# Optimization experiments

Hardware: AMD Instinct MI355X
Metric: run time of the kernel (lower is better)

## Reference

```python
import jax, jax.numpy as jnp
import numpy as np

D_IN = 1024
D_OUT = 1024
NUM_HEADS = 16
HEAD_DIM = D_OUT // NUM_HEADS


def setup_inputs() -> dict:
    key = jax.random.key(0)
    ks = jax.random.split(key, 6)
    s = 1.0 / np.sqrt(D_IN)
    inputs = jax.random.normal(ks[0], (4, 2048, D_IN), dtype=jnp.float32)
    Wq = jax.random.uniform(ks[1], (D_IN, D_OUT), jnp.float32, -s, s)
    Wk = jax.random.uniform(ks[2], (D_IN, D_OUT), jnp.float32, -s, s)
    Wv = jax.random.uniform(ks[3], (D_IN, D_OUT), jnp.float32, -s, s)
    so = 1.0 / np.sqrt(D_OUT)
    Wo = jax.random.uniform(ks[4], (D_OUT, D_OUT), jnp.float32, -so, so)
    bo = jax.random.uniform(ks[5], (D_OUT,), jnp.float32, -so, so)
    return {"inputs": inputs, "Wq": Wq, "Wk": Wk, "Wv": Wv, "Wo": Wo, "bo": bo}


def reference(inputs, Wq, Wk, Wv, Wo, bo):
    b, n, _ = inputs.shape
    # projections -> [b, h, n, d]
    def split_heads(x):
        return x.reshape(b, n, NUM_HEADS, HEAD_DIM).transpose(0, 2, 1, 3)
    q = split_heads(inputs @ Wq)
    k = split_heads(inputs @ Wk)
    v = split_heads(inputs @ Wv)
    scores = jnp.einsum('bhqd,bhkd->bhqk', q, k) / np.sqrt(HEAD_DIM).astype(np.float32)
    causal = jnp.tril(jnp.ones((n, n), dtype=bool))  # True = keep
    scores = jnp.where(causal, scores, -jnp.inf)
    weights = jax.nn.softmax(scores, axis=-1)
    ctx = jnp.einsum('bhqk,bhkd->bhqd', weights, v)
    ctx = ctx.transpose(0, 2, 1, 3).reshape(b, n, D_OUT)
    return ctx @ Wo + bo
```

## Files before the change

### kernel.cpp

```cpp
#include <hip/hip_runtime.h>

typedef unsigned short u16;
typedef unsigned int u32;
typedef __attribute__((ext_vector_type(8))) short short8;
typedef __attribute__((ext_vector_type(4))) float floatx4;
typedef __attribute__((ext_vector_type(4))) unsigned short ushort4_t;
typedef __attribute__((ext_vector_type(4))) float float4_t;
typedef __attribute__((ext_vector_type(2))) unsigned int uint2_t;


__device__ __forceinline__ u16 f2bf(float f) {
  unsigned u = __builtin_bit_cast(unsigned, f);
  u += 0x7FFFu + ((u >> 16) & 1u);
  return (u16)(u >> 16);
}

__device__ __forceinline__ u32 pack_bf2(float a, float b) {
  u32 ua = __builtin_bit_cast(u32, a) + 0x8000u;
  u32 ub = __builtin_bit_cast(u32, b) + 0x8000u;
  return __builtin_amdgcn_perm(ua, ub, 0x07060302u);
}

__device__ __forceinline__ void gload_lds16(const void* g, void* l) {
  __builtin_amdgcn_global_load_lds(
      (const __attribute__((address_space(1))) void*)g,
      (__attribute__((address_space(3))) void*)l, 16, 0, 0);
}


__global__ void cvt_x(const float* __restrict__ src, u16* __restrict__ dst) {
  int i = blockIdx.x * 256 + threadIdx.x;
  float4_t f = ((const float4_t*)src)[i];
  ushort4_t u;
  u.x = f2bf(f.x); u.y = f2bf(f.y); u.z = f2bf(f.z); u.w = f2bf(f.w);
  ((ushort4_t*)dst)[i] = u;
}

__global__ __launch_bounds__(256) void transpose_cvt4(
    const float* __restrict__ wq, const float* __restrict__ wk,
    const float* __restrict__ wv, const float* __restrict__ wo,
    u16* __restrict__ qk, u16* __restrict__ vt, u16* __restrict__ ot, float sc) {
  __shared__ float T[64][65];
  const int which = blockIdx.z;
  const float* s = (which == 0) ? wq : (which == 1) ? wk : (which == 2) ? wv : wo;
  u16* d = (which == 0) ? qk : (which == 1) ? (qk + (1u << 20)) : (which == 2) ? vt : ot;
  const float scale = (which == 0) ? sc : 1.f;
  const int n0 = blockIdx.x * 64, k0 = blockIdx.y * 64;
  const int c = threadIdx.x & 63, rg = threadIdx.x >> 6;
  for (int i = 0; i < 16; ++i) {
    int r = i * 4 + rg;
    T[r][c] = s[(k0 + r) * 1024 + n0 + c];
  }
  __syncthreads();
  for (int i = 0; i < 16; ++i) {
    int r = i * 4 + rg;
    d[(n0 + r) * 1024 + k0 + c] = f2bf(T[c][r] * scale);
  }
}

template <int MODE>
__global__ __launch_bounds__(256) void gemm_bt(
    const u16* __restrict__ A, const u16* __restrict__ Bt, void* __restrict__ Cv,
    const float* __restrict__ bias, int K, int lda, int ldb, int ldc) {
  __shared__ u16 As[2][128 * 32];
  __shared__ u16 Bs[2][128 * 32];
  const int tid = threadIdx.x;
  const int w = tid >> 6, l = tid & 63, quad = l >> 4, l16 = l & 15;
  const int wm = w >> 1, wn = w & 1;
  const size_t m0 = (size_t)blockIdx.y * 128, n0 = (size_t)blockIdx.x * 128;

  floatx4 acc[4][4];
  for (int i = 0; i < 4; ++i)
    for (int j = 0; j < 4; ++j) acc[i][j] = (floatx4){0.f, 0.f, 0.f, 0.f};

  auto stage = [&](int k0, int buf) {
    for (int i = 0; i < 2; ++i) {
      int c = i * 256 + tid;
      int row = c >> 2, off = (c & 3) * 8;
      gload_lds16(A + (m0 + row) * (size_t)lda + k0 + off, &As[buf][c * 8]);
      gload_lds16(Bt + (n0 + row) * (size_t)ldb + k0 + off, &Bs[buf][c * 8]);
    }
  };

  const int nk = K >> 5;
  stage(0, 0);
  __syncthreads();

  for (int ki = 0; ki < nk; ++ki) {
    const int buf = ki & 1;
    if (ki + 1 < nk) stage((ki + 1) << 5, buf ^ 1);

    short8 a[4], bb[4];
    for (int im = 0; im < 4; ++im)
      a[im] = *(const short8*)&As[buf][(wm * 64 + im * 16 + l16) * 32 + quad * 8];
    for (int in = 0; in < 4; ++in)
      bb[in] = *(const short8*)&Bs[buf][(wn * 64 + in * 16 + l16) * 32 + quad * 8];
    for (int im = 0; im < 4; ++im)
      for (int in = 0; in < 4; ++in)
        acc[im][in] = __builtin_amdgcn_mfma_f32_16x16x32_bf16(a[im], bb[in], acc[im][in], 0, 0, 0);

    __syncthreads();
  }

  for (int im = 0; im < 4; ++im)
    for (int in = 0; in < 4; ++in) {
      size_t r0 = m0 + wm * 64 + im * 16 + quad * 4;
      size_t col = n0 + wn * 64 + in * 16 + l16;
      float bv = (MODE == 1) ? bias[col] : 0.f;
      for (int r = 0; r < 4; ++r) {
        float val = acc[im][in][r] + bv;
        if (MODE == 0)
          ((u16*)Cv)[(r0 + r) * (size_t)ldc + col] = f2bf(val);
        else
          ((float*)Cv)[(r0 + r) * (size_t)ldc + col] = val;
      }
    }
}

__global__ __launch_bounds__(256) void flash_attn(
    const u16* __restrict__ QK, const u16* __restrict__ Vt, u16* __restrict__ ctx) {
  __shared__ u16 Ks[2][64 * 64];
  __shared__ u16 Vs[2][64 * 64];
  __shared__ u16 Ps[4 * 16 * 64];
  __shared__ float Ls[128];

  const int tid = threadIdx.x;
  const int w = tid >> 6, l = tid & 63, quad = l >> 4, l16 = l & 15;
  const int bh = blockIdx.x, qt = 15 - (int)blockIdx.y;
  const int b = bh >> 4, h = bh & 15;
  const int q0w = qt * 128 + w * 32;
  const int nkt = 2 * qt + 2;
  const int ktmax_w = (q0w + 31) >> 6;
  const int xr = (l16 & 7) << 4;

  auto stage = [&](int kt, int buf) {
    for (int i = 0; i < 2; ++i) {
      int c = i * 256 + tid;
      int row = c >> 3, scol = ((c & 7) ^ (row & 7)) << 3;
      gload_lds16(QK + (size_t)(b * 2048 + kt * 64 + row) * 2048 + 1024 + h * 64 + scol,
                  &Ks[buf][c * 8]);
      gload_lds16(Vt + (size_t)(h * 64 + row) * 8192 + b * 2048 + kt * 64 + scol,
                  &Vs[buf][c * 8]);
    }
  };

  short8 aq[2][2];
  for (int qf = 0; qf < 2; ++qf) {
    const size_t base = (size_t)(b * 2048 + q0w + qf * 16 + l16) * 2048 + h * 64 + quad * 8;
    aq[qf][0] = *(const short8*)(QK + base);
    aq[qf][1] = *(const short8*)(QK + base + 32);
  }

  floatx4 o[2][4];
  float lsum[2] = {0.f, 0.f};
  for (int qf = 0; qf < 2; ++qf)
    for (int df = 0; df < 4; ++df) o[qf][df] = (floatx4){0.f, 0.f, 0.f, 0.f};

  char* Psw = (char*)Ps + w * 2048;

  stage(0, 0);
  __syncthreads();

  for (int kt = 0; kt < nkt; ++kt) {
    const int buf = kt & 1;
    if (kt + 1 < nkt) stage(kt + 1, buf ^ 1);

    if (kt <= ktmax_w) {
      const bool need_mask = (kt == ktmax_w);

      short8 ka[4][2], bv[4][2];
      for (int nf = 0; nf < 4; ++nf) {
        const char* kb = (const char*)&Ks[buf][0] + (nf * 16 + l16) * 128;
        ka[nf][0] = *(const short8*)(kb + ((quad * 16) ^ xr));
        ka[nf][1] = *(const short8*)(kb + ((64 + quad * 16) ^ xr));
      }
      for (int df = 0; df < 4; ++df) {
        const char* vb = (const char*)&Vs[buf][0] + (df * 16 + l16) * 128;
        bv[df][0] = *(const short8*)(vb + ((quad * 16) ^ xr));
        bv[df][1] = *(const short8*)(vb + ((64 + quad * 16) ^ xr));
      }

      for (int qf = 0; qf < 2; ++qf) {
        floatx4 s[4];
        for (int nf = 0; nf < 4; ++nf) s[nf] = (floatx4){0.f, 0.f, 0.f, 0.f};
        for (int nf = 0; nf < 4; ++nf) {
          s[nf] = __builtin_amdgcn_mfma_f32_16x16x32_bf16(ka[nf][0], aq[qf][0], s[nf], 0, 0, 0);
          s[nf] = __builtin_amdgcn_mfma_f32_16x16x32_bf16(ka[nf][1], aq[qf][1], s[nf], 0, 0, 0);
        }
        if (need_mask) {
          int qpos = q0w + qf * 16 + l16;
          for (int nf = 0; nf < 4; ++nf)
            for (int r = 0; r < 4; ++r) {
              int kpos = kt * 64 + nf * 16 + quad * 4 + r;
              if (kpos > qpos) s[nf][r] = -1e30f;
            }
        }
        for (int nf = 0; nf < 4; ++nf) {
          float p0 = __builtin_amdgcn_exp2f(s[nf][0]);
          float p1 = __builtin_amdgcn_exp2f(s[nf][1]);
          float p2 = __builtin_amdgcn_exp2f(s[nf][2]);
          float p3 = __builtin_amdgcn_exp2f(s[nf][3]);
          lsum[qf] += (p0 + p1) + (p2 + p3);
          uint2_t pk;
          pk.x = pack_bf2(p1, p0);
          pk.y = pack_bf2(p3, p2);
          *(uint2_t*)(Psw + l16 * 128 + ((nf * 32 + quad * 8) ^ xr)) = pk;
        }
        for (int kk = 0; kk < 2; ++kk) {
          short8 ap = *(const short8*)(Psw + l16 * 128 + ((kk * 64 + quad * 16) ^ xr));
          for (int df = 0; df < 4; ++df)
            o[qf][df] = __builtin_amdgcn_mfma_f32_16x16x32_bf16(ap, bv[df][kk], o[qf][df], 0, 0, 0);
        }
      }
    }
    __syncthreads();
  }

  for (int qf = 0; qf < 2; ++qf) {
    float t = lsum[qf];
    t += __shfl_xor(t, 16, 64);
    t += __shfl_xor(t, 32, 64);
    if (l < 16) Ls[w * 32 + qf * 16 + l16] = __builtin_amdgcn_rcpf(t);
  }
  for (int qf = 0; qf < 2; ++qf) {
    floatx4 inv = *(const floatx4*)&Ls[w * 32 + qf * 16 + quad * 4];
    for (int df = 0; df < 4; ++df)
      for (int r = 0; r < 4; ++r) {
        float val = o[qf][df][r] * inv[r];
        size_t row = (size_t)(b * 2048 + q0w + qf * 16 + quad * 4 + r);
        ctx[row * 1024 + h * 64 + df * 16 + l16] = f2bf(val);
      }
  }
}


extern "C" void kernel_launch(void* const* d_in, const int* in_sizes, int n_in,
                              void* d_out, int out_size, void* d_ws, size_t ws_size,
                              hipStream_t stream) {
  const float* X  = (const float*)d_in[0];
  const float* Wq = (const float*)d_in[1];
  const float* Wk = (const float*)d_in[2];
  const float* Wv = (const float*)d_in[3];
  const float* Wo = (const float*)d_in[4];
  const float* bo = (const float*)d_in[5];

  char* ws = (char*)d_ws;
  u16* Xb   = (u16*)(ws);
  u16* WqkT = (u16*)(ws + (16u << 20));
  u16* WvT  = (u16*)(ws + (20u << 20));
  u16* WoT  = (u16*)(ws + (22u << 20));
  u16* QKb  = (u16*)(ws + (24u << 20));
  u16* Vt   = (u16*)(ws + (56u << 20));

  const float SC = 0.125f * 1.44269504088896340736f;

  cvt_x<<<8192, 256, 0, stream>>>(X, Xb);
  transpose_cvt4<<<dim3(16, 16, 4), 256, 0, stream>>>(Wq, Wk, Wv, Wo, WqkT, WvT, WoT, SC);

  gemm_bt<0><<<dim3(16, 64), 256, 0, stream>>>(Xb, WqkT, QKb, nullptr, 1024, 1024, 1024, 2048);
  gemm_bt<0><<<dim3(64, 8), 256, 0, stream>>>(WvT, Xb, Vt, nullptr, 1024, 1024, 1024, 8192);

  flash_attn<<<dim3(64, 16), 256, 0, stream>>>(QKb, Vt, Xb);

  gemm_bt<1><<<dim3(8, 64), 256, 0, stream>>>(Xb, WoT, (float*)d_out, bo, 1024, 1024, 1024, 1024);
}
```

Before: 268.8 us.

## Pair causal query tiles per block and keep P in registers for PV

Each attention block now processes two query tiles (qt and 15-qt) back to back, so every block does the same amount of causal work, and the grid is halved. The P matrix no longer round-trips through shared memory. The PV product now uses 16x16x16 MFMAs fed directly from the packed exp registers, with V fragments read as 4-element vectors, and the per-row normalisation is done with shuffles instead of LDS. This removes LDS traffic and load imbalance, at the cost of issuing twice as many smaller MFMAs for PV and a launch_bounds occupancy hint.

```diff
diff --git a/kernel.cpp b/kernel.cpp
--- a/kernel.cpp
+++ b/kernel.cpp
@@ -3,6 +3,7 @@
 typedef unsigned short u16;
 typedef unsigned int u32;
 typedef __attribute__((ext_vector_type(8))) short short8;
+typedef __attribute__((ext_vector_type(4))) short short4_t;
 typedef __attribute__((ext_vector_type(4))) float floatx4;
 typedef __attribute__((ext_vector_type(4))) unsigned short ushort4_t;
 typedef __attribute__((ext_vector_type(4))) float float4_t;
@@ -117,21 +118,19 @@
     }
 }
 
-__global__ __launch_bounds__(256) void flash_attn(
+__global__ __launch_bounds__(256, 2) void flash_attn(
     const u16* __restrict__ QK, const u16* __restrict__ Vt, u16* __restrict__ ctx) {
   __shared__ u16 Ks[2][64 * 64];
   __shared__ u16 Vs[2][64 * 64];
-  __shared__ u16 Ps[4 * 16 * 64];
-  __shared__ float Ls[128];
 
   const int tid = threadIdx.x;
   const int w = tid >> 6, l = tid & 63, quad = l >> 4, l16 = l & 15;
-  const int bh = blockIdx.x, qt = 15 - (int)blockIdx.y;
+  const int bh = blockIdx.x, p = blockIdx.y;
   const int b = bh >> 4, h = bh & 15;
-  const int q0w = qt * 128 + w * 32;
-  const int nkt = 2 * qt + 2;
-  const int ktmax_w = (q0w + 31) >> 6;
   const int xr = (l16 & 7) << 4;
+
+  const int qtA = 15 - p, qtB = p;
+  const int nktA = 2 * qtA + 2, ntot = nktA + 2 * qtB + 2;
 
   auto stage = [&](int kt, int buf) {
     for (int i = 0; i < 2; ++i) {
@@ -145,39 +144,64 @@
   };
 
   short8 aq[2][2];
-  for (int qf = 0; qf < 2; ++qf) {
-    const size_t base = (size_t)(b * 2048 + q0w + qf * 16 + l16) * 2048 + h * 64 + quad * 8;
-    aq[qf][0] = *(const short8*)(QK + base);
-    aq[qf][1] = *(const short8*)(QK + base + 32);
-  }
-
   floatx4 o[2][4];
-  float lsum[2] = {0.f, 0.f};
-  for (int qf = 0; qf < 2; ++qf)
-    for (int df = 0; df < 4; ++df) o[qf][df] = (floatx4){0.f, 0.f, 0.f, 0.f};
-
-  char* Psw = (char*)Ps + w * 2048;
-
+  float lsum[2];
+
+  auto load_q = [&](int q0w) {
+    for (int qf = 0; qf < 2; ++qf) {
+      const size_t base = (size_t)(b * 2048 + q0w + qf * 16 + l16) * 2048 + h * 64 + quad * 8;
+      aq[qf][0] = *(const short8*)(QK + base);
+      aq[qf][1] = *(const short8*)(QK + base + 32);
+    }
+    for (int qf = 0; qf < 2; ++qf) {
+      lsum[qf] = 0.f;
+      for (int df = 0; df < 4; ++df) o[qf][df] = (floatx4){0.f, 0.f, 0.f, 0.f};
+    }
+  };
+
+  auto epilogue = [&](int q0w) {
+    for (int qf = 0; qf < 2; ++qf) {
+      float t = lsum[qf];
+      t += __shfl_xor(t, 16, 64);
+      t += __shfl_xor(t, 32, 64);
+      float inv = __builtin_amdgcn_rcpf(t);
+      size_t row = (size_t)(b * 2048 + q0w + qf * 16 + l16);
+      for (int df = 0; df < 4; ++df) {
+        ushort4_t st;
+        for (int r = 0; r < 4; ++r) st[r] = f2bf(o[qf][df][r] * inv);
+        *(ushort4_t*)(ctx + row * 1024 + h * 64 + df * 16 + quad * 4) = st;
+      }
+    }
+  };
+
+  int q0w = qtA * 128 + w * 32;
+  int ktmax_w = (q0w + 31) >> 6;
+  load_q(q0w);
   stage(0, 0);
   __syncthreads();
 
-  for (int kt = 0; kt < nkt; ++kt) {
-    const int buf = kt & 1;
-    if (kt + 1 < nkt) stage(kt + 1, buf ^ 1);
+  for (int t = 0; t < ntot; ++t) {
+    const int buf = t & 1;
+    const int kt = (t < nktA) ? t : t - nktA;
+    if (t + 1 < ntot) {
+      int tn = t + 1;
+      stage((tn < nktA) ? tn : tn - nktA, buf ^ 1);
+    }
 
     if (kt <= ktmax_w) {
       const bool need_mask = (kt == ktmax_w);
 
-      short8 ka[4][2], bv[4][2];
+      short8 ka[4][2];
       for (int nf = 0; nf < 4; ++nf) {
         const char* kb = (const char*)&Ks[buf][0] + (nf * 16 + l16) * 128;
         ka[nf][0] = *(const short8*)(kb + ((quad * 16) ^ xr));
         ka[nf][1] = *(const short8*)(kb + ((64 + quad * 16) ^ xr));
       }
+      short4_t va[4][4];
       for (int df = 0; df < 4; ++df) {
         const char* vb = (const char*)&Vs[buf][0] + (df * 16 + l16) * 128;
-        bv[df][0] = *(const short8*)(vb + ((quad * 16) ^ xr));
-        bv[df][1] = *(const short8*)(vb + ((64 + quad * 16) ^ xr));
+        for (int nf = 0; nf < 4; ++nf)
+          va[nf][df] = *(const short4_t*)(vb + ((nf * 32 + quad * 8) ^ xr));
       }
 
       for (int qf = 0; qf < 2; ++qf) {
@@ -204,33 +228,22 @@
           uint2_t pk;
           pk.x = pack_bf2(p1, p0);
           pk.y = pack_bf2(p3, p2);
-          *(uint2_t*)(Psw + l16 * 128 + ((nf * 32 + quad * 8) ^ xr)) = pk;
+          short4_t pb = __builtin_bit_cast(short4_t, pk);
+          for (int df = 0; df < 4; ++df)
+            o[qf][df] = __builtin_amdgcn_mfma_f32_16x16x16bf16_1k(va[nf][df], pb, o[qf][df], 0, 0, 0);
         }
-        for (int kk = 0; kk < 2; ++kk) {
-          short8 ap = *(const short8*)(Psw + l16 * 128 + ((kk * 64 + quad * 16) ^ xr));
-          for (int df = 0; df < 4; ++df)
-            o[qf][df] = __builtin_amdgcn_mfma_f32_16x16x32_bf16(ap, bv[df][kk], o[qf][df], 0, 0, 0);
-        }
       }
     }
     __syncthreads();
-  }
-
-  for (int qf = 0; qf < 2; ++qf) {
-    float t = lsum[qf];
-    t += __shfl_xor(t, 16, 64);
-    t += __shfl_xor(t, 32, 64);
-    if (l < 16) Ls[w * 32 + qf * 16 + l16] = __builtin_amdgcn_rcpf(t);
-  }
-  for (int qf = 0; qf < 2; ++qf) {
-    floatx4 inv = *(const floatx4*)&Ls[w * 32 + qf * 16 + quad * 4];
-    for (int df = 0; df < 4; ++df)
-      for (int r = 0; r < 4; ++r) {
-        float val = o[qf][df][r] * inv[r];
-        size_t row = (size_t)(b * 2048 + q0w + qf * 16 + quad * 4 + r);
-        ctx[row * 1024 + h * 64 + df * 16 + l16] = f2bf(val);
-      }
-  }
+
+    if (t == nktA - 1) {
+      epilogue(q0w);
+      q0w = qtB * 128 + w * 32;
+      ktmax_w = (q0w + 31) >> 6;
+      load_q(q0w);
+    }
+  }
+  epilogue(q0w);
 }
 
 
@@ -260,7 +273,7 @@
   gemm_bt<0><<<dim3(16, 64), 256, 0, stream>>>(Xb, WqkT, QKb, nullptr, 1024, 1024, 1024, 2048);
   gemm_bt<0><<<dim3(64, 8), 256, 0, stream>>>(WvT, Xb, Vt, nullptr, 1024, 1024, 1024, 8192);
 
-  flash_attn<<<dim3(64, 16), 256, 0, stream>>>(QKb, Vt, Xb);
+  flash_attn<<<dim3(64, 8), 256, 0, stream>>>(QKb, Vt, Xb);
 
   gemm_bt<1><<<dim3(8, 64), 256, 0, stream>>>(Xb, WoT, (float*)d_out, bo, 1024, 1024, 1024, 1024);
 }
```

Result: faster. 261.5 us (-2.7%).

## Keep softmax probabilities in registers and feed PV MFMA directly

Applied to the files above, without the earlier changes.

Removes the per-wave LDS round trip for the P matrix by feeding the packed bf16 probabilities straight into a 16x16x16 MFMA as the B operand. V is loaded from LDS as four-element fragments, and the output is computed transposed so the epilogue can write ushort4 vectors without the shared normalization buffer. It also issues the first K/V stage earlier and adds a min-blocks-per-CU hint of 4. In exchange the PV product uses twice as many smaller MFMAs, and the launch-bounds hint may force register spills.

```diff
diff --git a/kernel.cpp b/kernel.cpp
--- a/kernel.cpp
+++ b/kernel.cpp
@@ -3,6 +3,7 @@
 typedef unsigned short u16;
 typedef unsigned int u32;
 typedef __attribute__((ext_vector_type(8))) short short8;
+typedef __attribute__((ext_vector_type(4))) short short4_t;
 typedef __attribute__((ext_vector_type(4))) float floatx4;
 typedef __attribute__((ext_vector_type(4))) unsigned short ushort4_t;
 typedef __attribute__((ext_vector_type(4))) float float4_t;
@@ -117,21 +118,20 @@
     }
 }
 
-__global__ __launch_bounds__(256) void flash_attn(
+__global__ __launch_bounds__(256, 4) void flash_attn(
     const u16* __restrict__ QK, const u16* __restrict__ Vt, u16* __restrict__ ctx) {
   __shared__ u16 Ks[2][64 * 64];
   __shared__ u16 Vs[2][64 * 64];
-  __shared__ u16 Ps[4 * 16 * 64];
-  __shared__ float Ls[128];
 
   const int tid = threadIdx.x;
   const int w = tid >> 6, l = tid & 63, quad = l >> 4, l16 = l & 15;
   const int bh = blockIdx.x, qt = 15 - (int)blockIdx.y;
   const int b = bh >> 4, h = bh & 15;
+  const int xr = (l16 & 7) << 4;
+
   const int q0w = qt * 128 + w * 32;
   const int nkt = 2 * qt + 2;
   const int ktmax_w = (q0w + 31) >> 6;
-  const int xr = (l16 & 7) << 4;
 
   auto stage = [&](int kt, int buf) {
     for (int i = 0; i < 2; ++i) {
@@ -144,6 +144,8 @@
     }
   };
 
+  stage(0, 0);
+
   short8 aq[2][2];
   for (int qf = 0; qf < 2; ++qf) {
     const size_t base = (size_t)(b * 2048 + q0w + qf * 16 + l16) * 2048 + h * 64 + quad * 8;
@@ -156,9 +158,6 @@
   for (int qf = 0; qf < 2; ++qf)
     for (int df = 0; df < 4; ++df) o[qf][df] = (floatx4){0.f, 0.f, 0.f, 0.f};
 
-  char* Psw = (char*)Ps + w * 2048;
-
-  stage(0, 0);
   __syncthreads();
 
   for (int kt = 0; kt < nkt; ++kt) {
@@ -168,16 +167,17 @@
     if (kt <= ktmax_w) {
       const bool need_mask = (kt == ktmax_w);
 
-      short8 ka[4][2], bv[4][2];
+      short8 ka[4][2];
       for (int nf = 0; nf < 4; ++nf) {
         const char* kb = (const char*)&Ks[buf][0] + (nf * 16 + l16) * 128;
         ka[nf][0] = *(const short8*)(kb + ((quad * 16) ^ xr));
         ka[nf][1] = *(const short8*)(kb + ((64 + quad * 16) ^ xr));
       }
+      short4_t va[4][4];
       for (int df = 0; df < 4; ++df) {
         const char* vb = (const char*)&Vs[buf][0] + (df * 16 + l16) * 128;
-        bv[df][0] = *(const short8*)(vb + ((quad * 16) ^ xr));
-        bv[df][1] = *(const short8*)(vb + ((64 + quad * 16) ^ xr));
+        for (int nf = 0; nf < 4; ++nf)
+          va[nf][df] = *(const short4_t*)(vb + ((nf * 32 + quad * 8) ^ xr));
       }
 
       for (int qf = 0; qf < 2; ++qf) {
@@ -204,12 +204,9 @@
           uint2_t pk;
           pk.x = pack_bf2(p1, p0);
           pk.y = pack_bf2(p3, p2);
-          *(uint2_t*)(Psw + l16 * 128 + ((nf * 32 + quad * 8) ^ xr)) = pk;
-        }
-        for (int kk = 0; kk < 2; ++kk) {
-          short8 ap = *(const short8*)(Psw + l16 * 128 + ((kk * 64 + quad * 16) ^ xr));
+          short4_t pb = __builtin_bit_cast(short4_t, pk);
           for (int df = 0; df < 4; ++df)
-            o[qf][df] = __builtin_amdgcn_mfma_f32_16x16x32_bf16(ap, bv[df][kk], o[qf][df], 0, 0, 0);
+            o[qf][df] = __builtin_amdgcn_mfma_f32_16x16x16bf16_1k(va[nf][df], pb, o[qf][df], 0, 0, 0);
         }
       }
     }
@@ -220,16 +217,13 @@
     float t = lsum[qf];
     t += __shfl_xor(t, 16, 64);
     t += __shfl_xor(t, 32, 64);
-    if (l < 16) Ls[w * 32 + qf * 16 + l16] = __builtin_amdgcn_rcpf(t);
-  }
-  for (int qf = 0; qf < 2; ++qf) {
-    floatx4 inv = *(const floatx4*)&Ls[w * 32 + qf * 16 + quad * 4];
-    for (int df = 0; df < 4; ++df)
-      for (int r = 0; r < 4; ++r) {
-        float val = o[qf][df][r] * inv[r];
-        size_t row = (size_t)(b * 2048 + q0w + qf * 16 + quad * 4 + r);
-        ctx[row * 1024 + h * 64 + df * 16 + l16] = f2bf(val);
-      }
+    float inv = __builtin_amdgcn_rcpf(t);
+    size_t row = (size_t)(b * 2048 + q0w + qf * 16 + l16);
+    for (int df = 0; df < 4; ++df) {
+      ushort4_t st;
+      for (int r = 0; r < 4; ++r) st[r] = f2bf(o[qf][df][r] * inv);
+      *(ushort4_t*)(ctx + row * 1024 + h * 64 + df * 16 + quad * 4) = st;
+    }
   }
 }
 
```

Measured after the change: 421.9 us. 1.57x slower.
